# Optimization experiments

Measured on AMD Instinct MI355X. Metric: run time of the kernel, lower is better.

## Reference

```python
import jax, jax.numpy as jnp
import numpy as np

K = 3
EPS = 1e-08
N_SRC = 65536   # source points
M_QRY = 262144  # query points
C_FEAT = 128


def setup_inputs() -> dict:
    key = jax.random.key(0)
    k1, k2, k3, k4 = jax.random.split(key, 4)
    s_feats = jax.random.normal(k1, (N_SRC, C_FEAT), dtype=jnp.float32)
    q_points = jax.random.normal(k2, (M_QRY, 3), dtype=jnp.float32)
    s_points = jax.random.normal(k3, (N_SRC, 3), dtype=jnp.float32)
    neighbor_indices = jax.random.randint(k4, (M_QRY, K), 0, N_SRC, dtype=jnp.int64)
    return {
        "s_feats": s_feats,
        "q_points": q_points,
        "s_points": s_points,
        "neighbor_indices": neighbor_indices,
    }


def reference(s_feats, q_points, s_points, neighbor_indices):
    # k-NN inverse-distance interpolation (k > 1 branch of KNNInterpolate)
    knn_idx = neighbor_indices[:, :K]            # [M, k]
    knn_points = s_points[knn_idx]               # [M, k, 3] gather
    knn_feats = s_feats[knn_idx]                 # [M, k, C] gather
    # squared distances query -> each neighbor
    d2 = jnp.sum((q_points[:, None, :] - knn_points) ** 2, axis=-1)  # [M, k]
    w = 1.0 / (d2 + EPS)                          # inverse-distance weights
    w = w / jnp.sum(w, axis=-1, keepdims=True)    # normalize over k
    q_feats = jnp.einsum("mk,mkc->mc", w, knn_feats)  # weighted reduction
    return q_feats
```

## Files before the change

kernel.cpp:

```cpp
#include <hip/hip_runtime.h>

#define KNN_EPS 1e-8f
#define C_FEAT 128
#define N_SRC 65536
#define M_QRY 262144
#define QPT 2

typedef float f4 __attribute__((ext_vector_type(4)));
typedef _Float16 h4 __attribute__((ext_vector_type(4)));

__global__ __launch_bounds__(256) void cvt_feats_kernel(
    const float* __restrict__ s_feats, _Float16* __restrict__ ws)
{
    const int t = blockIdx.x * blockDim.x + threadIdx.x;
    const f4 a = ((const f4*)s_feats)[t];
    const h4 h = __builtin_convertvector(a, h4);
    __builtin_nontemporal_store(h, (h4*)ws + t);
}

__global__ __launch_bounds__(256) void knn_interp_kernel(
    const _Float16* __restrict__ feats16,
    const float* __restrict__ q_points,
    const float* __restrict__ s_points,
    const int*   __restrict__ nbr_idx,
    float* __restrict__ out)
{
    const int t  = blockIdx.x * blockDim.x + threadIdx.x;
    const int g  = t >> 5;
    const int c4 = t & 31;
    const int mbase = g * QPT;

    int idx[QPT][3];
#pragma unroll
    for (int q = 0; q < QPT; ++q)
#pragma unroll
        for (int k = 0; k < 3; ++k)
            idx[q][k] = nbr_idx[(mbase + q) * 3 + k];

    h4 v[QPT][3];
#pragma unroll
    for (int q = 0; q < QPT; ++q)
#pragma unroll
        for (int k = 0; k < 3; ++k)
            v[q][k] = ((const h4*)(feats16 + (size_t)idx[q][k] * C_FEAT))[c4];

    float w[QPT][3];
#pragma unroll
    for (int q = 0; q < QPT; ++q) {
        const int m = mbase + q;
        const float qx = q_points[m * 3 + 0];
        const float qy = q_points[m * 3 + 1];
        const float qz = q_points[m * 3 + 2];
#pragma unroll
        for (int k = 0; k < 3; ++k) {
            const int s = idx[q][k];
            const float dx = qx - s_points[s * 3 + 0];
            const float dy = qy - s_points[s * 3 + 1];
            const float dz = qz - s_points[s * 3 + 2];
            w[q][k] = __builtin_amdgcn_rcpf(dx * dx + dy * dy + dz * dz + KNN_EPS);
        }
    }

#pragma unroll
    for (int q = 0; q < QPT; ++q) {
        const float inv = __builtin_amdgcn_rcpf(w[q][0] + w[q][1] + w[q][2]);
        const f4 r = (w[q][0] * inv) * __builtin_convertvector(v[q][0], f4)
                   + (w[q][1] * inv) * __builtin_convertvector(v[q][1], f4)
                   + (w[q][2] * inv) * __builtin_convertvector(v[q][2], f4);
        __builtin_nontemporal_store(r, (f4*)(out + (size_t)(mbase + q) * C_FEAT) + c4);
    }
}

extern "C" void kernel_launch(void* const* d_in, const int* in_sizes, int n_in,
                              void* d_out, int out_size, void* d_ws, size_t ws_size,
                              hipStream_t stream) {
    const float* s_feats  = (const float*)d_in[0];
    const float* q_points = (const float*)d_in[1];
    const float* s_points = (const float*)d_in[2];
    const int*   nbr_idx  = (const int*)d_in[3];
    float* out = (float*)d_out;
    _Float16* feats16 = (_Float16*)d_ws;

    {
        const int total = N_SRC * C_FEAT / 4;
        cvt_feats_kernel<<<total / 256, 256, 0, stream>>>(s_feats, feats16);
    }

    {
        const int total_threads = M_QRY * 32 / QPT;
        const int grid = total_threads / 256;
        knn_interp_kernel<<<grid, 256, 0, stream>>>(feats16, q_points, s_points,
                                                    nbr_idx, out);
    }
}
```

Baseline: 204.4 us.

## Compute KNN weights once per query in shared memory, use 16-byte gathers

```diff
diff --git a/kernel.cpp b/kernel.cpp
--- a/kernel.cpp
+++ b/kernel.cpp
@@ -4,10 +4,12 @@
 #define C_FEAT 128
 #define N_SRC 65536
 #define M_QRY 262144
-#define QPT 2
+#define QBLK 16
 
-typedef float f4 __attribute__((ext_vector_type(4)));
+typedef float    f4 __attribute__((ext_vector_type(4)));
+typedef float    f8 __attribute__((ext_vector_type(8)));
 typedef _Float16 h4 __attribute__((ext_vector_type(4)));
+typedef _Float16 h8 __attribute__((ext_vector_type(8)));
 
 __global__ __launch_bounds__(256) void cvt_feats_kernel(
     const float* __restrict__ s_feats, _Float16* __restrict__ ws)
@@ -25,50 +27,44 @@
     const int*   __restrict__ nbr_idx,
     float* __restrict__ out)
 {
-    const int t  = blockIdx.x * blockDim.x + threadIdx.x;
-    const int g  = t >> 5;
-    const int c4 = t & 31;
-    const int mbase = g * QPT;
+    __shared__ int   s_i[QBLK][3];
+    __shared__ float s_wt[QBLK][3];
 
-    int idx[QPT][3];
-#pragma unroll
-    for (int q = 0; q < QPT; ++q)
-#pragma unroll
-        for (int k = 0; k < 3; ++k)
-            idx[q][k] = nbr_idx[(mbase + q) * 3 + k];
+    const int tid    = threadIdx.x;
+    const int mblock = blockIdx.x * QBLK;
 
-    h4 v[QPT][3];
-#pragma unroll
-    for (int q = 0; q < QPT; ++q)
-#pragma unroll
-        for (int k = 0; k < 3; ++k)
-            v[q][k] = ((const h4*)(feats16 + (size_t)idx[q][k] * C_FEAT))[c4];
+    if (tid < QBLK * 3) {
+        const int q = tid / 3;
+        const int k = tid - q * 3;
+        const int m = mblock + q;
+        const int s = nbr_idx[m * 3 + k];
+        const float dx = q_points[m * 3 + 0] - s_points[s * 3 + 0];
+        const float dy = q_points[m * 3 + 1] - s_points[s * 3 + 1];
+        const float dz = q_points[m * 3 + 2] - s_points[s * 3 + 2];
+        s_i[q][k]  = s;
+        s_wt[q][k] = __builtin_amdgcn_rcpf(dx * dx + dy * dy + dz * dz + KNN_EPS);
+    }
+    __syncthreads();
 
-    float w[QPT][3];
-#pragma unroll
-    for (int q = 0; q < QPT; ++q) {
-        const int m = mbase + q;
-        const float qx = q_points[m * 3 + 0];
-        const float qy = q_points[m * 3 + 1];
-        const float qz = q_points[m * 3 + 2];
-#pragma unroll
-        for (int k = 0; k < 3; ++k) {
-            const int s = idx[q][k];
-            const float dx = qx - s_points[s * 3 + 0];
-            const float dy = qy - s_points[s * 3 + 1];
-            const float dz = qz - s_points[s * 3 + 2];
-            w[q][k] = __builtin_amdgcn_rcpf(dx * dx + dy * dy + dz * dz + KNN_EPS);
-        }
-    }
+    const int q = tid >> 4;
+    const int l = tid & 15;
+    const int m = mblock + q;
 
-#pragma unroll
-    for (int q = 0; q < QPT; ++q) {
-        const float inv = __builtin_amdgcn_rcpf(w[q][0] + w[q][1] + w[q][2]);
-        const f4 r = (w[q][0] * inv) * __builtin_convertvector(v[q][0], f4)
-                   + (w[q][1] * inv) * __builtin_convertvector(v[q][1], f4)
-                   + (w[q][2] * inv) * __builtin_convertvector(v[q][2], f4);
-        __builtin_nontemporal_store(r, (f4*)(out + (size_t)(mbase + q) * C_FEAT) + c4);
-    }
+    const float w0 = s_wt[q][0], w1 = s_wt[q][1], w2 = s_wt[q][2];
+    const float inv = __builtin_amdgcn_rcpf(w0 + w1 + w2);
+    const int i0 = s_i[q][0], i1 = s_i[q][1], i2 = s_i[q][2];
+
+    const h8 v0 = ((const h8*)(feats16 + (size_t)i0 * C_FEAT))[l];
+    const h8 v1 = ((const h8*)(feats16 + (size_t)i1 * C_FEAT))[l];
+    const h8 v2 = ((const h8*)(feats16 + (size_t)i2 * C_FEAT))[l];
+
+    const f8 r = (w0 * inv) * __builtin_convertvector(v0, f8)
+               + (w1 * inv) * __builtin_convertvector(v1, f8)
+               + (w2 * inv) * __builtin_convertvector(v2, f8);
+
+    float* o = out + (size_t)m * C_FEAT + l * 8;
+    __builtin_nontemporal_store(__builtin_shufflevector(r, r, 0, 1, 2, 3), (f4*)o);
+    __builtin_nontemporal_store(__builtin_shufflevector(r, r, 4, 5, 6, 7), (f4*)(o + 4));
 }
 
 extern "C" void kernel_launch(void* const* d_in, const int* in_sizes, int n_in,
@@ -87,8 +83,7 @@
     }
 
     {
-        const int total_threads = M_QRY * 32 / QPT;
-        const int grid = total_threads / 256;
+        const int grid = M_QRY / QBLK;
         knn_interp_kernel<<<grid, 256, 0, stream>>>(feats16, q_points, s_points,
                                                     nbr_idx, out);
     }
```

Result: faster. 197.4 us (-3.4%).
